# Kernel tuning notes

Measured on AMD Instinct MI355X. Metric: run time of the kernel, lower is better.

The kernel has to match this reference:

```python
import jax, jax.numpy as jnp
import numpy as np

NUM_STREAM = 4
SINKHORN_ITERS = 20
HC_EPS = 1e-06
NORM_EPS = 1e-06


def sinkhorn_knopps(h, iters, eps):
    # h: [B, S, ns, ns]
    h = jax.nn.softmax(h, axis=-1) + eps
    h = h / (h.sum(-2, keepdims=True) + eps)
    for _ in range(iters - 1):  # fixed small trip count (19), unrolled
        h = h / (h.sum(-1, keepdims=True) + eps)
        h = h / (h.sum(-2, keepdims=True) + eps)
    return h


def setup_inputs() -> dict:
    key = jax.random.key(0)
    k1, k2, k3, k4 = jax.random.split(key, 4)
    B, S, ns, H = 4, 2048, NUM_STREAM, 1024
    mix_hc = (2 + ns) * ns  # 24
    x = jax.random.normal(k1, (B, S, ns, H), dtype=jnp.float32)
    hc_fn = jax.random.normal(k2, (mix_hc, ns * H), dtype=jnp.float32) * 0.02
    hc_scale = jax.random.uniform(k3, (3,), dtype=jnp.float32)
    hc_base = jax.random.normal(k4, (mix_hc,), dtype=jnp.float32)
    return {"x": x, "hc_fn": hc_fn, "hc_scale": hc_scale, "hc_base": hc_base}


def reference(x, hc_fn, hc_scale, hc_base):
    B, S, ns, H = x.shape
    xf = x.reshape(B, S, ns * H).astype(jnp.float32)
    # RMSNorm stats (applied as a post-scale on the linear output, as in source)
    rsqrt = jax.lax.rsqrt(jnp.mean(jnp.square(xf), axis=-1, keepdims=True) + NORM_EPS)
    weight = jnp.einsum('bsd,md->bsm', xf, hc_fn) * rsqrt  # [B, S, mix_hc]
    h_pre = weight[..., :ns]
    h_post = weight[..., ns:2 * ns]
    h_res = weight[..., 2 * ns:].reshape(B, S, ns, ns)
    h_pre = jax.nn.sigmoid(h_pre * hc_scale[0] + hc_base[:ns][None, None, :]) + HC_EPS
    h_post = 2.0 * jax.nn.sigmoid(h_post * hc_scale[1] + hc_base[ns:2 * ns][None, None, :])
    h_res = h_res * hc_scale[2] + hc_base[2 * ns:].reshape(ns, ns)[None, None, :, :]
    h_res = sinkhorn_knopps(h_res, SINKHORN_ITERS, HC_EPS)
    xs = xf.reshape(B, S, ns, H)
    # hc_pre: mix streams into a single vector per token
    y = jnp.einsum('bsn,bsnh->bsh', h_pre, xs)  # [B, S, H]
    # hc_post: broadcast gated y back to streams + Sinkhorn-mixed residual streams
    out = h_post[..., None] * y[:, :, None, :] + jnp.einsum('bsij,bsih->bsjh', h_res, xs)
    return out.astype(x.dtype)
```

## Files before the change

### kernel.cpp

```cpp
#include <hip/hip_runtime.h>
#include <math.h>

#define NS 4
#define HDIM 1024
#define DDIM 4096
#define TOK_B 16
#define KCH 256
#define NCH 16
#define NPS 4
#define HC_EPS_F 1e-6f
#define NORM_EPS_F 1e-6f

typedef __attribute__((ext_vector_type(8))) short short8;
typedef __attribute__((ext_vector_type(4))) float f32x4;

__device__ __forceinline__ float frcp(float v) { return __builtin_amdgcn_rcpf(v); }

__device__ __forceinline__ void gload_lds16(const float* g, float* l) {
  __builtin_amdgcn_global_load_lds(
      (const __attribute__((address_space(1))) void*)g,
      (__attribute__((address_space(3))) void*)l, 16, 0, 0);
}

#define CVT_PAIR(j, f0, f1)                                                     \
  { unsigned p0 = __float_as_uint(f0), p1 = __float_as_uint(f1);                \
    H.u[j] = (p1 & 0xFFFF0000u) | (p0 >> 16);                                   \
    unsigned q0 = __float_as_uint((f0) - __uint_as_float(p0 & 0xFFFF0000u));    \
    unsigned q1 = __float_as_uint((f1) - __uint_as_float(p1 & 0xFFFF0000u));    \
    L.u[j] = (q1 & 0xFFFF0000u) | (q0 >> 16); }

__device__ __forceinline__ void cvt_hl(const float4 a, const float4 b,
                                       short8& hi, short8& lo) {
  union { unsigned u[4]; short8 s; } H, L;
  CVT_PAIR(0, a.x, a.y)
  CVT_PAIR(1, a.z, a.w)
  CVT_PAIR(2, b.x, b.y)
  CVT_PAIR(3, b.z, b.w)
  hi = H.s; lo = L.s;
}

__launch_bounds__(256, 4)
__global__ void mhc_convb(const float* __restrict__ hc_fn,
                          unsigned short* __restrict__ bh,
                          unsigned short* __restrict__ bl) {
  const int g = blockIdx.x * 256 + threadIdx.x;
  const float4 v = ((const float4*)hc_fn)[g];
  ushort4 h, l;
  unsigned p;
  p = __float_as_uint(v.x); h.x = p >> 16; l.x = __float_as_uint(v.x - __uint_as_float(p & 0xFFFF0000u)) >> 16;
  p = __float_as_uint(v.y); h.y = p >> 16; l.y = __float_as_uint(v.y - __uint_as_float(p & 0xFFFF0000u)) >> 16;
  p = __float_as_uint(v.z); h.z = p >> 16; l.z = __float_as_uint(v.z - __uint_as_float(p & 0xFFFF0000u)) >> 16;
  p = __float_as_uint(v.w); h.w = p >> 16; l.w = __float_as_uint(v.w - __uint_as_float(p & 0xFFFF0000u)) >> 16;
  ((ushort4*)bh)[g] = h;
  ((ushort4*)bl)[g] = l;
}

__launch_bounds__(256, 2)
__global__ void mhc_dots_mfma(const float* __restrict__ x,
                              const unsigned short* __restrict__ bh,
                              const unsigned short* __restrict__ bl,
                              float* __restrict__ wp, int ntok) {
  __shared__ float xs[2][TOK_B * KCH];
  const int tid  = threadIdx.x;
  const int lane = tid & 63;
  const int wave = tid >> 6;
  const long long tok0 = (long long)blockIdx.x * TOK_B;

#define STAGE(d, kcn)                                                           \
  {                                                                             \
    _Pragma("unroll")                                                           \
    for (int c = 0; c < 4; ++c) {                                               \
      const int t = c * 4 + wave;                                               \
      const int c4src = lane ^ (t & 7);                                         \
      gload_lds16(x + (tok0 + t) * DDIM + (kcn) * KCH + c4src * 4,              \
                  &xs[d][(c * 4 + wave) * KCH + lane * 4 - lane * 4 + (c * 256 + wave * 64) * 4]); \
    }                                                                           \
  }
#undef STAGE
#define STAGE(d, kcn)                                                           \
  {                                                                             \
    _Pragma("unroll")                                                           \
    for (int c = 0; c < 4; ++c) {                                               \
      const int S = c * 256 + wave * 64;                  \
      const int t = S >> 6;                                      \
      const int c4src = lane ^ (t & 7);                                         \
      gload_lds16(x + (tok0 + t) * DDIM + (kcn) * KCH + c4src * 4,              \
                  &xs[d][(size_t)S * 4]);                                       \
    }                                                                           \
  }

  const int kh  = wave;
  const int row = lane & 15;
  const int ks  = lane >> 4;

  const unsigned short* bp0h = bh + (long long)row * DDIM + kh * 64 + ks * 8;
  const unsigned short* bp0l = bl + (long long)row * DDIM + kh * 64 + ks * 8;
  const int fr1c = (row < 8) ? (16 + row) : 23;
  const unsigned short* bp1h = bh + (long long)fr1c * DDIM + kh * 64 + ks * 8;
  const unsigned short* bp1l = bl + (long long)fr1c * DDIM + kh * 64 + ks * 8;
  const bool v1 = (row < 8);
  const short8 z8 = {0, 0, 0, 0, 0, 0, 0, 0};

  f32x4 acc0 = {0.f, 0.f, 0.f, 0.f};
  f32x4 acc1 = {0.f, 0.f, 0.f, 0.f};
  float ssq = 0.f;

  STAGE(0, 0)
  __syncthreads();

  const int rsw = row & 7;
  const float* arow0 = xs[0] + (size_t)row * KCH;
  const float* arow1 = xs[1] + (size_t)row * KCH;

  for (int kc = 0; kc < NCH; ++kc) {
    if (kc < NCH - 1) {
      if (kc & 1) STAGE(0, kc + 1) else STAGE(1, kc + 1)
    }
    const float* arow = (kc & 1) ? arow1 : arow0;
    const int kb = kc * KCH;

    #pragma unroll
    for (int s = 0; s < 2; ++s) {
      const int ko = kb + s * 32;
      const short8 b0h = *(const short8*)(bp0h + ko);
      const short8 b0l = *(const short8*)(bp0l + ko);
      const short8 b1h = v1 ? *(const short8*)(bp1h + ko) : z8;
      const short8 b1l = v1 ? *(const short8*)(bp1l + ko) : z8;

      const int c4 = kh * 16 + s * 8 + ks * 2;
      const float4 a0 = *(const float4*)(arow + (size_t)(c4 ^ rsw) * 4);
      const float4 a1 = *(const float4*)(arow + (size_t)((c4 + 1) ^ rsw) * 4);

      ssq = fmaf(a0.x, a0.x, fmaf(a0.y, a0.y, fmaf(a0.z, a0.z, fmaf(a0.w, a0.w, ssq))));
      ssq = fmaf(a1.x, a1.x, fmaf(a1.y, a1.y, fmaf(a1.z, a1.z, fmaf(a1.w, a1.w, ssq))));

      short8 ahi, alo;
      cvt_hl(a0, a1, ahi, alo);

      acc0 = __builtin_amdgcn_mfma_f32_16x16x32_bf16(ahi, b0h, acc0, 0, 0, 0);
      acc1 = __builtin_amdgcn_mfma_f32_16x16x32_bf16(ahi, b1h, acc1, 0, 0, 0);
      acc0 = __builtin_amdgcn_mfma_f32_16x16x32_bf16(ahi, b0l, acc0, 0, 0, 0);
      acc1 = __builtin_amdgcn_mfma_f32_16x16x32_bf16(ahi, b1l, acc1, 0, 0, 0);
      acc0 = __builtin_amdgcn_mfma_f32_16x16x32_bf16(alo, b0h, acc0, 0, 0, 0);
      acc1 = __builtin_amdgcn_mfma_f32_16x16x32_bf16(alo, b1h, acc1, 0, 0, 0);
    }
    __syncthreads();
  }

  ssq += __shfl_xor(ssq, 16, 64);
  ssq += __shfl_xor(ssq, 32, 64);

  float* wpk = wp + (long long)kh * ntok * 25;
  if (lane < 16) wpk[(tok0 + lane) * 25 + 24] = ssq;
  const int rq = lane >> 4;
  #pragma unroll
  for (int r = 0; r < 4; ++r)
    wpk[(tok0 + rq * 4 + r) * 25 + row] = acc0[r];
  if (row < 8) {
    #pragma unroll
    for (int r = 0; r < 4; ++r)
      wpk[(tok0 + rq * 4 + r) * 25 + 16 + row] = acc1[r];
  }
#undef STAGE
}

__launch_bounds__(256, 4)
__global__ void mhc_sinkhorn(const float* __restrict__ wp,
                             const float* __restrict__ hc_scale,
                             const float* __restrict__ hc_base,
                             float* __restrict__ gates, int ntok) {
  const int lane = threadIdx.x & 63;
  const int wave = threadIdx.x >> 6;
  const long long tok = (long long)blockIdx.x * 16 + wave * 4 + (lane >> 4);
  const int e = lane & 15;

  const long long kstride = (long long)ntok * 25;
  const float* b = wp + tok * 25;
  float sres = 0.f, ssq = 0.f, spre = 0.f, spost = 0.f;
  #pragma unroll
  for (int ps = 0; ps < NPS; ++ps) {
    const float* p = b + ps * kstride;
    sres += p[8 + e];
    ssq  += p[24];
    if (e < NS) { spre += p[e]; spost += p[NS + e]; }
  }

  const float rs = rsqrtf(ssq * (1.0f / DDIM) + NORM_EPS_F);
  const float s0 = hc_scale[0], s1 = hc_scale[1], s2 = hc_scale[2];

  float h = sres * rs * s2 + hc_base[8 + e];
  float mx = fmaxf(h, __shfl_xor(h, 1, 4));
  mx = fmaxf(mx, __shfl_xor(mx, 2, 4));
  float ex = expf(h - mx);
  float sm = ex + __shfl_xor(ex, 1, 4);
  sm += __shfl_xor(sm, 2, 4);
  h = ex * frcp(sm) + HC_EPS_F;
  float cs = h + __shfl_xor(h, 4, 16);
  cs += __shfl_xor(cs, 8, 16);
  h *= frcp(cs + HC_EPS_F);
  #pragma unroll 1
  for (int itn = 0; itn < 19; ++itn) {
    float rsum = h + __shfl_xor(h, 1, 4);
    rsum += __shfl_xor(rsum, 2, 4);
    h *= frcp(rsum + HC_EPS_F);
    float csum = h + __shfl_xor(h, 4, 16);
    csum += __shfl_xor(csum, 8, 16);
    h *= frcp(csum + HC_EPS_F);
  }
  float* g = gates + tok * 24;
  g[8 + e] = h;
  if (e < NS) {
    g[e] = frcp(1.0f + expf(-(spre * rs * s0 + hc_base[e]))) + HC_EPS_F;
    g[NS + e] = 2.0f * frcp(1.0f + expf(-(spost * rs * s1 + hc_base[NS + e])));
  }
}

__launch_bounds__(256, 8)
__global__ void mhc_out(const float* __restrict__ x,
                        const float* __restrict__ gates,
                        float* __restrict__ out) {
  const long long token = blockIdx.x;
  const int q = threadIdx.x;

  const float* g = gates + token * 24;
  float hp[NS], hq[NS], hr[NS][NS];
  #pragma unroll
  for (int i = 0; i < NS; ++i) {
    hp[i] = g[i];
    hq[i] = g[NS + i];
    #pragma unroll
    for (int j = 0; j < NS; ++j) hr[i][j] = g[8 + i * NS + j];
  }

  const float4* xb = (const float4*)(x + token * DDIM);
  float4 xv[NS];
  #pragma unroll
  for (int i = 0; i < NS; ++i) xv[i] = xb[i * 256 + q];

  float4 y;
  y.x = hp[0]*xv[0].x + hp[1]*xv[1].x + hp[2]*xv[2].x + hp[3]*xv[3].x;
  y.y = hp[0]*xv[0].y + hp[1]*xv[1].y + hp[2]*xv[2].y + hp[3]*xv[3].y;
  y.z = hp[0]*xv[0].z + hp[1]*xv[1].z + hp[2]*xv[2].z + hp[3]*xv[3].z;
  y.w = hp[0]*xv[0].w + hp[1]*xv[1].w + hp[2]*xv[2].w + hp[3]*xv[3].w;

  float4* ob = (float4*)(out + token * DDIM);
  #pragma unroll
  for (int n = 0; n < NS; ++n) {
    float4 o;
    o.x = hq[n]*y.x + hr[0][n]*xv[0].x + hr[1][n]*xv[1].x + hr[2][n]*xv[2].x + hr[3][n]*xv[3].x;
    o.y = hq[n]*y.y + hr[0][n]*xv[0].y + hr[1][n]*xv[1].y + hr[2][n]*xv[2].y + hr[3][n]*xv[3].y;
    o.z = hq[n]*y.z + hr[0][n]*xv[0].z + hr[1][n]*xv[1].z + hr[2][n]*xv[2].z + hr[3][n]*xv[3].z;
    o.w = hq[n]*y.w + hr[0][n]*xv[0].w + hr[1][n]*xv[1].w + hr[2][n]*xv[2].w + hr[3][n]*xv[3].w;
    ob[n * 256 + q] = o;
  }
}

extern "C" void kernel_launch(void* const* d_in, const int* in_sizes, int n_in,
                              void* d_out, int out_size, void* d_ws, size_t ws_size,
                              hipStream_t stream) {
  const float* x        = (const float*)d_in[0];
  const float* hc_fn    = (const float*)d_in[1];
  const float* hc_scale = (const float*)d_in[2];
  const float* hc_base  = (const float*)d_in[3];
  float* out = (float*)d_out;

  const int ntok = in_sizes[0] / DDIM;
  float* gates = (float*)d_ws;

  float* wp = out;
  unsigned short* bh = (unsigned short*)(out + (size_t)NPS * ntok * 25);
  unsigned short* bl = bh + 24 * DDIM;

  mhc_convb<<<(24 * DDIM / 4) / 256, 256, 0, stream>>>(hc_fn, bh, bl);
  mhc_dots_mfma<<<ntok / TOK_B, 256, 0, stream>>>(x, bh, bl, wp, ntok);
  mhc_sinkhorn<<<ntok / 16, 256, 0, stream>>>(wp, hc_scale, hc_base, gates, ntok);
  mhc_out<<<ntok, 256, 0, stream>>>(x, gates, out);
}
```

Measured before the change: 96.88 us.

## Fuse Sinkhorn gating into the MFMA dots kernel and halve token block

Merges the dot-product kernel and the Sinkhorn/gate kernel into one. The per-wave partial sums now reduce in shared memory instead of round-tripping through a global scratch buffer, which also removes one launch. The token block shrinks from 16 to 8, so the 16-row MFMA tiles carry duplicated rows, but twice as many blocks are launched. Gates are written in a transposed [24][ntok] layout, and the output kernel reads them that way. The risk is wasted MFMA work on the duplicate rows and the Sinkhorn stage running serially after the dots inside each block.

```diff
diff --git a/kernel.cpp b/kernel.cpp
--- a/kernel.cpp
+++ b/kernel.cpp
@@ -4,10 +4,9 @@
 #define NS 4
 #define HDIM 1024
 #define DDIM 4096
-#define TOK_B 16
+#define TOK_B 8
 #define KCH 256
 #define NCH 16
-#define NPS 4
 #define HC_EPS_F 1e-6f
 #define NORM_EPS_F 1e-6f
 
@@ -56,11 +55,14 @@
 }
 
 __launch_bounds__(256, 2)
-__global__ void mhc_dots_mfma(const float* __restrict__ x,
-                              const unsigned short* __restrict__ bh,
-                              const unsigned short* __restrict__ bl,
-                              float* __restrict__ wp, int ntok) {
+__global__ void mhc_fused(const float* __restrict__ x,
+                          const unsigned short* __restrict__ bh,
+                          const unsigned short* __restrict__ bl,
+                          const float* __restrict__ hc_scale,
+                          const float* __restrict__ hc_base,
+                          float* __restrict__ gates, int ntok) {
   __shared__ float xs[2][TOK_B * KCH];
+  __shared__ float wsl[4][TOK_B][25];
   const int tid  = threadIdx.x;
   const int lane = tid & 63;
   const int wave = tid >> 6;
@@ -69,29 +71,19 @@
 #define STAGE(d, kcn)                                                           \
   {                                                                             \
     _Pragma("unroll")                                                           \
-    for (int c = 0; c < 4; ++c) {                                               \
-      const int t = c * 4 + wave;                                               \
-      const int c4src = lane ^ (t & 7);                                         \
-      gload_lds16(x + (tok0 + t) * DDIM + (kcn) * KCH + c4src * 4,              \
-                  &xs[d][(c * 4 + wave) * KCH + lane * 4 - lane * 4 + (c * 256 + wave * 64) * 4]); \
-    }                                                                           \
-  }
-#undef STAGE
-#define STAGE(d, kcn)                                                           \
-  {                                                                             \
-    _Pragma("unroll")                                                           \
-    for (int c = 0; c < 4; ++c) {                                               \
+    for (int c = 0; c < 2; ++c) {                                               \
       const int S = c * 256 + wave * 64;                  \
-      const int t = S >> 6;                                      \
+      const int t = S >> 6;                                 \
       const int c4src = lane ^ (t & 7);                                         \
       gload_lds16(x + (tok0 + t) * DDIM + (kcn) * KCH + c4src * 4,              \
                   &xs[d][(size_t)S * 4]);                                       \
     }                                                                           \
   }
 
-  const int kh  = wave;
-  const int row = lane & 15;
-  const int ks  = lane >> 4;
+  const int kh   = wave;
+  const int row  = lane & 15;
+  const int trow = row & 7;
+  const int ks   = lane >> 4;
 
   const unsigned short* bp0h = bh + (long long)row * DDIM + kh * 64 + ks * 8;
   const unsigned short* bp0l = bl + (long long)row * DDIM + kh * 64 + ks * 8;
@@ -108,28 +100,26 @@
   STAGE(0, 0)
   __syncthreads();
 
-  const int rsw = row & 7;
-  const float* arow0 = xs[0] + (size_t)row * KCH;
-  const float* arow1 = xs[1] + (size_t)row * KCH;
+  const float* arow0 = xs[0] + (size_t)trow * KCH;
+  const float* arow1 = xs[1] + (size_t)trow * KCH;
 
   for (int kc = 0; kc < NCH; ++kc) {
     if (kc < NCH - 1) {
       if (kc & 1) STAGE(0, kc + 1) else STAGE(1, kc + 1)
     }
     const float* arow = (kc & 1) ? arow1 : arow0;
-    const int kb = kc * KCH;
 
     #pragma unroll
     for (int s = 0; s < 2; ++s) {
-      const int ko = kb + s * 32;
+      const int ko = kc * KCH + s * 32;
       const short8 b0h = *(const short8*)(bp0h + ko);
       const short8 b0l = *(const short8*)(bp0l + ko);
       const short8 b1h = v1 ? *(const short8*)(bp1h + ko) : z8;
       const short8 b1l = v1 ? *(const short8*)(bp1l + ko) : z8;
 
       const int c4 = kh * 16 + s * 8 + ks * 2;
-      const float4 a0 = *(const float4*)(arow + (size_t)(c4 ^ rsw) * 4);
-      const float4 a1 = *(const float4*)(arow + (size_t)((c4 + 1) ^ rsw) * 4);
+      const float4 a0 = *(const float4*)(arow + (size_t)((c4) ^ trow) * 4);
+      const float4 a1 = *(const float4*)(arow + (size_t)((c4 + 1) ^ trow) * 4);
 
       ssq = fmaf(a0.x, a0.x, fmaf(a0.y, a0.y, fmaf(a0.z, a0.z, fmaf(a0.w, a0.w, ssq))));
       ssq = fmaf(a1.x, a1.x, fmaf(a1.y, a1.y, fmaf(a1.z, a1.z, fmaf(a1.w, a1.w, ssq))));
@@ -146,90 +136,80 @@
     }
     __syncthreads();
   }
-
+#undef STAGE
+
+  const int rq = lane >> 4;
+  if (rq < 2) {
+    #pragma unroll
+    for (int r = 0; r < 4; ++r) wsl[kh][rq * 4 + r][row] = acc0[r];
+    if (row < 8) {
+      #pragma unroll
+      for (int r = 0; r < 4; ++r) wsl[kh][rq * 4 + r][16 + row] = acc1[r];
+    }
+  }
   ssq += __shfl_xor(ssq, 16, 64);
   ssq += __shfl_xor(ssq, 32, 64);
-
-  float* wpk = wp + (long long)kh * ntok * 25;
-  if (lane < 16) wpk[(tok0 + lane) * 25 + 24] = ssq;
-  const int rq = lane >> 4;
-  #pragma unroll
-  for (int r = 0; r < 4; ++r)
-    wpk[(tok0 + rq * 4 + r) * 25 + row] = acc0[r];
-  if (row < 8) {
-    #pragma unroll
-    for (int r = 0; r < 4; ++r)
-      wpk[(tok0 + rq * 4 + r) * 25 + 16 + row] = acc1[r];
-  }
-#undef STAGE
-}
-
-__launch_bounds__(256, 4)
-__global__ void mhc_sinkhorn(const float* __restrict__ wp,
-                             const float* __restrict__ hc_scale,
-                             const float* __restrict__ hc_base,
-                             float* __restrict__ gates, int ntok) {
-  const int lane = threadIdx.x & 63;
-  const int wave = threadIdx.x >> 6;
-  const long long tok = (long long)blockIdx.x * 16 + wave * 4 + (lane >> 4);
-  const int e = lane & 15;
-
-  const long long kstride = (long long)ntok * 25;
-  const float* b = wp + tok * 25;
-  float sres = 0.f, ssq = 0.f, spre = 0.f, spost = 0.f;
-  #pragma unroll
-  for (int ps = 0; ps < NPS; ++ps) {
-    const float* p = b + ps * kstride;
-    sres += p[8 + e];
-    ssq  += p[24];
-    if (e < NS) { spre += p[e]; spost += p[NS + e]; }
-  }
-
-  const float rs = rsqrtf(ssq * (1.0f / DDIM) + NORM_EPS_F);
-  const float s0 = hc_scale[0], s1 = hc_scale[1], s2 = hc_scale[2];
-
-  float h = sres * rs * s2 + hc_base[8 + e];
-  float mx = fmaxf(h, __shfl_xor(h, 1, 4));
-  mx = fmaxf(mx, __shfl_xor(mx, 2, 4));
-  float ex = expf(h - mx);
-  float sm = ex + __shfl_xor(ex, 1, 4);
-  sm += __shfl_xor(sm, 2, 4);
-  h = ex * frcp(sm) + HC_EPS_F;
-  float cs = h + __shfl_xor(h, 4, 16);
-  cs += __shfl_xor(cs, 8, 16);
-  h *= frcp(cs + HC_EPS_F);
-  #pragma unroll 1
-  for (int itn = 0; itn < 19; ++itn) {
-    float rsum = h + __shfl_xor(h, 1, 4);
-    rsum += __shfl_xor(rsum, 2, 4);
-    h *= frcp(rsum + HC_EPS_F);
-    float csum = h + __shfl_xor(h, 4, 16);
-    csum += __shfl_xor(csum, 8, 16);
-    h *= frcp(csum + HC_EPS_F);
-  }
-  float* g = gates + tok * 24;
-  g[8 + e] = h;
-  if (e < NS) {
-    g[e] = frcp(1.0f + expf(-(spre * rs * s0 + hc_base[e]))) + HC_EPS_F;
-    g[NS + e] = 2.0f * frcp(1.0f + expf(-(spost * rs * s1 + hc_base[NS + e])));
+  if (ks == 0 && row < 8) wsl[kh][row][24] = ssq;
+  __syncthreads();
+
+  if (wave < 2) {
+    const int tt = wave * 4 + (lane >> 4);
+    const int e  = lane & 15;
+    float sres = wsl[0][tt][8 + e] + wsl[1][tt][8 + e] + wsl[2][tt][8 + e] + wsl[3][tt][8 + e];
+    float ssqt = wsl[0][tt][24] + wsl[1][tt][24] + wsl[2][tt][24] + wsl[3][tt][24];
+    float spre = 0.f, spost = 0.f;
+    if (e < NS) {
+      spre  = wsl[0][tt][e] + wsl[1][tt][e] + wsl[2][tt][e] + wsl[3][tt][e];
+      spost = wsl[0][tt][NS + e] + wsl[1][tt][NS + e] + wsl[2][tt][NS + e] + wsl[3][tt][NS + e];
+    }
+
+    const float rs = rsqrtf(ssqt * (1.0f / DDIM) + NORM_EPS_F);
+    const float s0 = hc_scale[0], s1 = hc_scale[1], s2 = hc_scale[2];
+
+    float h = sres * rs * s2 + hc_base[8 + e];
+    float mx = fmaxf(h, __shfl_xor(h, 1, 4));
+    mx = fmaxf(mx, __shfl_xor(mx, 2, 4));
+    float ex = expf(h - mx);
+    float sm = ex + __shfl_xor(ex, 1, 4);
+    sm += __shfl_xor(sm, 2, 4);
+    h = ex * frcp(sm) + HC_EPS_F;
+    float cs = h + __shfl_xor(h, 4, 16);
+    cs += __shfl_xor(cs, 8, 16);
+    h *= frcp(cs + HC_EPS_F);
+    #pragma unroll 1
+    for (int itn = 0; itn < 19; ++itn) {
+      float rsum = h + __shfl_xor(h, 1, 4);
+      rsum += __shfl_xor(rsum, 2, 4);
+      h *= frcp(rsum + HC_EPS_F);
+      float csum = h + __shfl_xor(h, 4, 16);
+      csum += __shfl_xor(csum, 8, 16);
+      h *= frcp(csum + HC_EPS_F);
+    }
+    gates[(size_t)(8 + e) * ntok + tok0 + tt] = h;
+    if (e < NS) {
+      gates[(size_t)e * ntok + tok0 + tt] =
+          frcp(1.0f + expf(-(spre * rs * s0 + hc_base[e]))) + HC_EPS_F;
+      gates[(size_t)(NS + e) * ntok + tok0 + tt] =
+          2.0f * frcp(1.0f + expf(-(spost * rs * s1 + hc_base[NS + e])));
+    }
   }
 }
 
 __launch_bounds__(256, 8)
 __global__ void mhc_out(const float* __restrict__ x,
                         const float* __restrict__ gates,
-                        float* __restrict__ out) {
+                        float* __restrict__ out, int ntok) {
   const long long token = blockIdx.x;
   const int q = threadIdx.x;
 
-  const float* g = gates + token * 24;
   float hp[NS], hq[NS], hr[NS][NS];
   #pragma unroll
   for (int i = 0; i < NS; ++i) {
-    hp[i] = g[i];
-    hq[i] = g[NS + i];
+    hp[i] = gates[(size_t)i * ntok + token];
+    hq[i] = gates[(size_t)(NS + i) * ntok + token];
     #pragma unroll
-    for (int j = 0; j < NS; ++j) hr[i][j] = g[8 + i * NS + j];
+    for (int j = 0; j < NS; ++j)
+      hr[i][j] = gates[(size_t)(8 + i * NS + j) * ntok + token];
   }
 
   const float4* xb = (const float4*)(x + token * DDIM);
@@ -267,12 +247,10 @@
   const int ntok = in_sizes[0] / DDIM;
   float* gates = (float*)d_ws;
 
-  float* wp = out;
-  unsigned short* bh = (unsigned short*)(out + (size_t)NPS * ntok * 25);
+  unsigned short* bh = (unsigned short*)out;
   unsigned short* bl = bh + 24 * DDIM;
 
   mhc_convb<<<(24 * DDIM / 4) / 256, 256, 0, stream>>>(hc_fn, bh, bl);
-  mhc_dots_mfma<<<ntok / TOK_B, 256, 0, stream>>>(x, bh, bl, wp, ntok);
-  mhc_sinkhorn<<<ntok / 16, 256, 0, stream>>>(wp, hc_scale, hc_base, gates, ntok);
-  mhc_out<<<ntok, 256, 0, stream>>>(x, gates, out);
-}
+  mhc_fused<<<ntok / TOK_B, 256, 0, stream>>>(x, bh, bl, hc_scale, hc_base, gates, ntok);
+  mhc_out<<<ntok, 256, 0, stream>>>(x, gates, out, ntok);
+}
```

Result: slower. 111.1 us (+14.7%).
